# Optimization experiments

Hardware: AMD Instinct MI355X
Metric: run time of the kernel (lower is better)

The kernel has to match this reference:

```python
import jax, jax.numpy as jnp
import numpy as np

MARGIN = 0.2
EPS = 1e-6  # torch.pairwise_distance default eps added to (x1 - x2)


def setup_inputs() -> dict:
    key = jax.random.key(0)
    k1, k2 = jax.random.split(key)
    N, D = 8192, 128
    x = jax.random.normal(k1, (N, D), dtype=jnp.float32)
    target = jax.random.randint(k2, (N,), 0, 1000)
    return {"x": x, "target": target}


def _pairwise_dist(x):
    # torch.pairwise_distance(x.unsqueeze(0), x.unsqueeze(1)):
    #   diff[i, j] = x[j] - x[i] + EPS ; dist[i, j] = ||diff[i, j]||_2
    # Expanded quadratic form avoids the [N, N, D] diff tensor:
    #   ||a - b + e||^2 = ||a||^2 + ||b||^2 - 2 a.b + 2e*sum(a - b) + D*e^2
    sq = jnp.sum(x * x, axis=1)          # [N]
    s = jnp.sum(x, axis=1)               # [N]
    dot = x @ x.T                        # [N, N]
    D = x.shape[1]
    d2 = (sq[None, :] + sq[:, None] - 2.0 * dot
          + 2.0 * EPS * (s[None, :] - s[:, None]) + D * EPS * EPS)
    return jnp.sqrt(jnp.maximum(d2, 0.0))


def reference(x, target):
    N = x.shape[0]
    dist = _pairwise_dist(x)                                 # [N, N]
    same = target[None, :] == target[:, None]                # [N, N] bool
    pos_mask = (same & ~jnp.eye(N, dtype=bool)).astype(x.dtype)
    hardest_pos = jnp.max(pos_mask * dist, axis=1, keepdims=True)  # [N, 1]
    neg_mask = (~same).astype(x.dtype)
    max_neg = jnp.max(dist, axis=1, keepdims=True)           # [N, 1]
    anchor_neg = dist + max_neg * (1.0 - neg_mask)           # push positives up
    hardest_neg = jnp.min(anchor_neg, axis=1, keepdims=True) # [N, 1]
    loss = jax.nn.relu(hardest_pos - hardest_neg + MARGIN)
    return jnp.mean(loss)
```

## Files before the change

kernel.cpp:

```cpp
#include <hip/hip_runtime.h>

#define N 8192
#define Dk 128
#define EPSC 1e-6f
#define MARGIN 0.2f

typedef __attribute__((ext_vector_type(8))) short bf16x8;
typedef __attribute__((ext_vector_type(4))) float f32x4;

__device__ __forceinline__ unsigned short f2bf(float f) {
    unsigned u = __float_as_uint(f);
    u = (u + 0x7FFFu + ((u >> 16) & 1u)) >> 16;
    return (unsigned short)u;
}

__global__ void prep_kernel(const float* __restrict__ x, const int* __restrict__ tgt,
                            uint4* __restrict__ Frag, uint2* __restrict__ QT,
                            float* __restrict__ P) {
    int wv = blockIdx.x * 4 + (threadIdx.x >> 6);
    int lane = threadIdx.x & 63;
    int row = wv * 4 + (lane >> 4);
    int c = lane & 15;
    const float4* x4 = reinterpret_cast<const float4*>(x);
    float4 v0 = x4[row * 32 + c * 2];
    float4 v1 = x4[row * 32 + c * 2 + 1];
    float sq = v0.x * v0.x + v0.y * v0.y + v0.z * v0.z + v0.w * v0.w +
               v1.x * v1.x + v1.y * v1.y + v1.z * v1.z + v1.w * v1.w;
    float s = v0.x + v0.y + v0.z + v0.w + v1.x + v1.y + v1.z + v1.w;
    ushort4 lo, hi;
    lo.x = f2bf(v0.x); lo.y = f2bf(v0.y); lo.z = f2bf(v0.z); lo.w = f2bf(v0.w);
    hi.x = f2bf(v1.x); hi.y = f2bf(v1.y); hi.z = f2bf(v1.z); hi.w = f2bf(v1.w);
    uint4 pk;
    pk.x = (unsigned)lo.x | ((unsigned)lo.y << 16);
    pk.y = (unsigned)lo.z | ((unsigned)lo.w << 16);
    pk.z = (unsigned)hi.x | ((unsigned)hi.y << 16);
    pk.w = (unsigned)hi.z | ((unsigned)hi.w << 16);
    Frag[((row >> 4) * 4 + (c >> 2)) * 64 + (c & 3) * 16 + (row & 15)] = pk;
#pragma unroll
    for (int m = 1; m <= 8; m <<= 1) {
        sq += __shfl_xor(sq, m);
        s += __shfl_xor(s, m);
    }
    if (c == 0) {
        P[row] = sq - 2.0f * EPSC * s;
        float Qj = sq + 2.0f * EPSC * s + (float)Dk * EPSC * EPSC;
        uint2 qt;
        qt.x = __float_as_uint(-0.5f * Qj);
        qt.y = (unsigned)tgt[row];
        QT[row] = qt;
    }
}

#define LOADB(Bb, qq, t)                              \
    do {                                              \
        const int jt_ = jt0 + (t);                    \
        Bb[0] = Fr[(jt_ * 4 + 0) * 64 + lane];        \
        Bb[1] = Fr[(jt_ * 4 + 1) * 64 + lane];        \
        Bb[2] = Fr[(jt_ * 4 + 2) * 64 + lane];        \
        Bb[3] = Fr[(jt_ * 4 + 3) * 64 + lane];        \
        qq = QT[jt_ * 16 + n];                        \
    } while (0)

#define COMPUTE(Bb, qq)                                                               \
    do {                                                                              \
        const float Qv_ = __uint_as_float(qq.x);                        \
        const int tv_ = (int)qq.y;                                                    \
        f32x4 acc[4];                                                                 \
        acc[0] = Qv_; acc[1] = Qv_; acc[2] = Qv_; acc[3] = Qv_;                       \
        _Pragma("unroll")                                                             \
        for (int kk = 0; kk < 4; ++kk) {                                              \
            _Pragma("unroll")                                                         \
            for (int ti = 0; ti < 4; ++ti)                                            \
                acc[ti] = __builtin_amdgcn_mfma_f32_16x16x32_bf16(Af[ti][kk], Bb[kk], \
                                                                  acc[ti], 0, 0, 0);  \
        }                                                                             \
        _Pragma("unroll")                                                             \
        for (int ti = 0; ti < 4; ++ti) {                                              \
            f32x4 v = acc[ti];                                                        \
            int e0 = tv_ == tsl[4 * ti + 0];                                          \
            int e1 = tv_ == tsl[4 * ti + 1];                                          \
            int e2 = tv_ == tsl[4 * ti + 2];                                          \
            int e3 = tv_ == tsl[4 * ti + 3];                                          \
            if (__ballot(e0 | e1 | e2 | e3)) {                                        \
                hp[4 * ti + 0] = fminf(hp[4 * ti + 0], e0 ? v[0] : INFINITY);         \
                hp[4 * ti + 1] = fminf(hp[4 * ti + 1], e1 ? v[1] : INFINITY);         \
                hp[4 * ti + 2] = fminf(hp[4 * ti + 2], e2 ? v[2] : INFINITY);         \
                hp[4 * ti + 3] = fminf(hp[4 * ti + 3], e3 ? v[3] : INFINITY);         \
                mn[4 * ti + 0] = fmaxf(mn[4 * ti + 0], e0 ? -INFINITY : v[0]);        \
                mn[4 * ti + 1] = fmaxf(mn[4 * ti + 1], e1 ? -INFINITY : v[1]);        \
                mn[4 * ti + 2] = fmaxf(mn[4 * ti + 2], e2 ? -INFINITY : v[2]);        \
                mn[4 * ti + 3] = fmaxf(mn[4 * ti + 3], e3 ? -INFINITY : v[3]);        \
            } else {                                                                  \
                mn[4 * ti + 0] = fmaxf(mn[4 * ti + 0], v[0]);                         \
                mn[4 * ti + 1] = fmaxf(mn[4 * ti + 1], v[1]);                         \
                mn[4 * ti + 2] = fmaxf(mn[4 * ti + 2], v[2]);                         \
                mn[4 * ti + 3] = fmaxf(mn[4 * ti + 3], v[3]);                         \
            }                                                                         \
        }                                                                             \
    } while (0)

__global__ __launch_bounds__(256, 2) void main_kernel(
        const uint4* __restrict__ Frag, const uint2* __restrict__ QT,
        const int* __restrict__ tgt,
        float* __restrict__ partHp, float* __restrict__ partMn) {
    const int w = threadIdx.x >> 6;
    const int lane = threadIdx.x & 63;
    const int n = lane & 15;
    const int q = lane >> 4;

    const int ig = (int)blockIdx.x >> 3;
    const int jg = (int)blockIdx.x & 7;
    const int rbase = ig * 64;
    const int jt0 = jg * 64 + w * 16;

    const bf16x8* Fr = reinterpret_cast<const bf16x8*>(Frag);

    bf16x8 Af[4][4];
#pragma unroll
    for (int ti = 0; ti < 4; ++ti)
#pragma unroll
        for (int kk = 0; kk < 4; ++kk)
            Af[ti][kk] = Fr[((ig * 4 + ti) * 4 + kk) * 64 + lane];

    int tsl[16];
#pragma unroll
    for (int ti = 0; ti < 4; ++ti) {
        int4 t4 = *reinterpret_cast<const int4*>(&tgt[rbase + 16 * ti + 4 * q]);
        tsl[4 * ti + 0] = t4.x;
        tsl[4 * ti + 1] = t4.y;
        tsl[4 * ti + 2] = t4.z;
        tsl[4 * ti + 3] = t4.w;
    }

    float hp[16], mn[16];
#pragma unroll
    for (int s = 0; s < 16; ++s) {
        hp[s] = INFINITY;
        mn[s] = -INFINITY;
    }

    bf16x8 Ba[4], Bb[4], Bc[4], Bd[4];
    uint2 qa, qb, qc, qd;

    LOADB(Ba, qa, 0);
    LOADB(Bb, qb, 1);
    LOADB(Bc, qc, 2);
    LOADB(Bd, qd, 3);
#pragma unroll
    for (int tt = 0; tt < 16; tt += 4) {
        COMPUTE(Ba, qa);
        if (tt < 12) LOADB(Ba, qa, tt + 4);
        COMPUTE(Bb, qb);
        if (tt < 12) LOADB(Bb, qb, tt + 5);
        COMPUTE(Bc, qc);
        if (tt < 12) LOADB(Bc, qc, tt + 6);
        COMPUTE(Bd, qd);
        if (tt < 12) LOADB(Bd, qd, tt + 7);
    }

#pragma unroll
    for (int m = 1; m <= 8; m <<= 1) {
#pragma unroll
        for (int s = 0; s < 16; ++s) {
            hp[s] = fminf(hp[s], __shfl_xor(hp[s], m));
            mn[s] = fmaxf(mn[s], __shfl_xor(mn[s], m));
        }
    }
    if (n == 0) {
        const int wg = jg * 4 + w;
#pragma unroll
        for (int ti = 0; ti < 4; ++ti)
#pragma unroll
            for (int r = 0; r < 4; ++r) {
                int i = rbase + 16 * ti + 4 * q + r;
                partHp[wg * N + i] = hp[4 * ti + r];
                partMn[wg * N + i] = mn[4 * ti + r];
            }
    }
}

__global__ void finish_kernel(const float* __restrict__ P,
                              const float* __restrict__ partHp,
                              const float* __restrict__ partMn,
                              float* __restrict__ out) {
    int i = blockIdx.x * 256 + threadIdx.x;
    float hpm = INFINITY, mnm = -INFINITY;
#pragma unroll
    for (int wg = 0; wg < 32; ++wg) {
        hpm = fminf(hpm, partHp[wg * N + i]);
        mnm = fmaxf(mnm, partMn[wg * N + i]);
    }
    float Pi = P[i];
    float hp = sqrtf(fmaxf(fmaf(-2.0f, hpm, Pi), 0.0f));
    float hn = sqrtf(fmaxf(fmaf(-2.0f, mnm, Pi), 0.0f));
    float sum = fmaxf(hp - hn + MARGIN, 0.0f) * (1.0f / (float)N);
#pragma unroll
    for (int m = 32; m >= 1; m >>= 1) sum += __shfl_xor(sum, m);
    __shared__ float ws[4];
    int lane = threadIdx.x & 63, wv = threadIdx.x >> 6;
    if (lane == 0) ws[wv] = sum;
    __syncthreads();
    if (threadIdx.x == 0) atomicAdd(out, ws[0] + ws[1] + ws[2] + ws[3]);
}

extern "C" void kernel_launch(void* const* d_in, const int* in_sizes, int n_in,
                              void* d_out, int out_size, void* d_ws, size_t ws_size,
                              hipStream_t stream) {
    const float* x = (const float*)d_in[0];
    const int* tgt = (const int*)d_in[1];
    float* out = (float*)d_out;

    char* ws = (char*)d_ws;
    const size_t frag_b = (size_t)N * Dk * 2;
    uint4* Frag = (uint4*)ws;
    uint2* QT = (uint2*)(ws + frag_b);
    float* P = (float*)(ws + frag_b + (size_t)N * 8);
    float* partHp = (float*)(ws + frag_b + (size_t)N * 12);
    float* partMn = (float*)(ws + frag_b + (size_t)N * 12 + (size_t)32 * N * 4);

    hipMemsetAsync(d_out, 0, sizeof(float), stream);
    prep_kernel<<<N / 16, 256, 0, stream>>>(x, tgt, Frag, QT, P);
    main_kernel<<<1024, 256, 0, stream>>>(Frag, QT, tgt, partHp, partMn);
    finish_kernel<<<32, 256, 0, stream>>>(P, partHp, partMn, out);
}
```

Measured before the change: 102.0 us.

## Sort rows by class so same-class checks run only on band tiles

Adds a counting sort of samples by target class (histogram, prefix scan, scatter) and permutes the rows when building the bf16 fragments. In the main kernel each 64-row block then knows the column range that holds its own classes and runs the per-element equality and hardest-positive path only for tiles that overlap that range. All other tiles do a plain max update, which removes the per-tile compares and ballots. The price is three extra small launches plus atomics, and the B-prefetch ring shrinks from four buffers to three.

```diff
diff --git a/kernel.cpp b/kernel.cpp
--- a/kernel.cpp
+++ b/kernel.cpp
@@ -2,6 +2,7 @@
 
 #define N 8192
 #define Dk 128
+#define NC 1024
 #define EPSC 1e-6f
 #define MARGIN 0.2f
 
@@ -14,16 +15,57 @@
     return (unsigned short)u;
 }
 
-__global__ void prep_kernel(const float* __restrict__ x, const int* __restrict__ tgt,
+__global__ void hist_kernel(const int* __restrict__ tgt, int* __restrict__ hist) {
+    int i = blockIdx.x * 256 + threadIdx.x;
+    atomicAdd(&hist[tgt[i]], 1);
+}
+
+__global__ void scan_kernel(const int* __restrict__ hist, int* __restrict__ pref,
+                            int* __restrict__ cursor) {
+    __shared__ int tmp[NC];
+    int t = threadIdx.x;
+    int h = hist[t];
+    tmp[t] = h;
+    __syncthreads();
+#pragma unroll
+    for (int off = 1; off < NC; off <<= 1) {
+        int v = (t >= off) ? tmp[t - off] : 0;
+        __syncthreads();
+        tmp[t] += v;
+        __syncthreads();
+    }
+    int ex = tmp[t] - h;
+    pref[t] = ex;
+    cursor[t] = ex;
+}
+
+__global__ void scatter_kernel(const int* __restrict__ tgt, const int* __restrict__ pref,
+                               const int* __restrict__ hist, int* __restrict__ cursor,
+                               int* __restrict__ perm, uint2* __restrict__ band,
+                               int* __restrict__ cls) {
+    int i = blockIdx.x * 256 + threadIdx.x;
+    int c = tgt[i];
+    int pos = atomicAdd(&cursor[c], 1);
+    perm[pos] = i;
+    uint2 b;
+    b.x = (unsigned)pref[c];
+    b.y = (unsigned)(pref[c] + hist[c]);
+    band[pos] = b;
+    cls[pos] = c;
+}
+
+__global__ void prep_kernel(const float* __restrict__ x, const int* __restrict__ perm,
+                            const int* __restrict__ cls,
                             uint4* __restrict__ Frag, uint2* __restrict__ QT,
                             float* __restrict__ P) {
     int wv = blockIdx.x * 4 + (threadIdx.x >> 6);
     int lane = threadIdx.x & 63;
-    int row = wv * 4 + (lane >> 4);
+    int k = wv * 4 + (lane >> 4);
     int c = lane & 15;
+    int orig = perm[k];
     const float4* x4 = reinterpret_cast<const float4*>(x);
-    float4 v0 = x4[row * 32 + c * 2];
-    float4 v1 = x4[row * 32 + c * 2 + 1];
+    float4 v0 = x4[orig * 32 + c * 2];
+    float4 v1 = x4[orig * 32 + c * 2 + 1];
     float sq = v0.x * v0.x + v0.y * v0.y + v0.z * v0.z + v0.w * v0.w +
                v1.x * v1.x + v1.y * v1.y + v1.z * v1.z + v1.w * v1.w;
     float s = v0.x + v0.y + v0.z + v0.w + v1.x + v1.y + v1.z + v1.w;
@@ -35,36 +77,35 @@
     pk.y = (unsigned)lo.z | ((unsigned)lo.w << 16);
     pk.z = (unsigned)hi.x | ((unsigned)hi.y << 16);
     pk.w = (unsigned)hi.z | ((unsigned)hi.w << 16);
-    Frag[((row >> 4) * 4 + (c >> 2)) * 64 + (c & 3) * 16 + (row & 15)] = pk;
+    Frag[((k >> 4) * 4 + (c >> 2)) * 64 + (c & 3) * 16 + (k & 15)] = pk;
 #pragma unroll
     for (int m = 1; m <= 8; m <<= 1) {
         sq += __shfl_xor(sq, m);
         s += __shfl_xor(s, m);
     }
     if (c == 0) {
-        P[row] = sq - 2.0f * EPSC * s;
+        P[k] = sq - 2.0f * EPSC * s;
         float Qj = sq + 2.0f * EPSC * s + (float)Dk * EPSC * EPSC;
         uint2 qt;
         qt.x = __float_as_uint(-0.5f * Qj);
-        qt.y = (unsigned)tgt[row];
-        QT[row] = qt;
-    }
-}
-
-#define LOADB(Bb, qq, t)                              \
-    do {                                              \
-        const int jt_ = jt0 + (t);                    \
-        Bb[0] = Fr[(jt_ * 4 + 0) * 64 + lane];        \
-        Bb[1] = Fr[(jt_ * 4 + 1) * 64 + lane];        \
-        Bb[2] = Fr[(jt_ * 4 + 2) * 64 + lane];        \
-        Bb[3] = Fr[(jt_ * 4 + 3) * 64 + lane];        \
-        qq = QT[jt_ * 16 + n];                        \
+        qt.y = (unsigned)cls[k];
+        QT[k] = qt;
+    }
+}
+
+#define LOADB(Bb, qq, t)                       \
+    do {                                       \
+        const int jt_ = jt0 + (t);             \
+        Bb[0] = Fr[(jt_ * 4 + 0) * 64 + lane]; \
+        Bb[1] = Fr[(jt_ * 4 + 1) * 64 + lane]; \
+        Bb[2] = Fr[(jt_ * 4 + 2) * 64 + lane]; \
+        Bb[3] = Fr[(jt_ * 4 + 3) * 64 + lane]; \
+        qq = QT[jt_ * 16 + n];                 \
     } while (0)
 
-#define COMPUTE(Bb, qq)                                                               \
+#define COMPUTE(Bb, qq, t)                                                            \
     do {                                                                              \
         const float Qv_ = __uint_as_float(qq.x);                        \
-        const int tv_ = (int)qq.y;                                                    \
         f32x4 acc[4];                                                                 \
         acc[0] = Qv_; acc[1] = Qv_; acc[2] = Qv_; acc[3] = Qv_;                       \
         _Pragma("unroll")                                                             \
@@ -74,14 +115,16 @@
                 acc[ti] = __builtin_amdgcn_mfma_f32_16x16x32_bf16(Af[ti][kk], Bb[kk], \
                                                                   acc[ti], 0, 0, 0);  \
         }                                                                             \
-        _Pragma("unroll")                                                             \
-        for (int ti = 0; ti < 4; ++ti) {                                              \
-            f32x4 v = acc[ti];                                                        \
-            int e0 = tv_ == tsl[4 * ti + 0];                                          \
-            int e1 = tv_ == tsl[4 * ti + 1];                                          \
-            int e2 = tv_ == tsl[4 * ti + 2];                                          \
-            int e3 = tv_ == tsl[4 * ti + 3];                                          \
-            if (__ballot(e0 | e1 | e2 | e3)) {                                        \
+        const int jc_ = (jt0 + (t)) * 16;                                             \
+        if (jc_ < bHi && jc_ + 16 > bLo) {      \
+            const int tv_ = (int)qq.y;                                                \
+            _Pragma("unroll")                                                         \
+            for (int ti = 0; ti < 4; ++ti) {                                          \
+                f32x4 v = acc[ti];                                                    \
+                int e0 = tv_ == tsl[4 * ti + 0];                                      \
+                int e1 = tv_ == tsl[4 * ti + 1];                                      \
+                int e2 = tv_ == tsl[4 * ti + 2];                                      \
+                int e3 = tv_ == tsl[4 * ti + 3];                                      \
                 hp[4 * ti + 0] = fminf(hp[4 * ti + 0], e0 ? v[0] : INFINITY);         \
                 hp[4 * ti + 1] = fminf(hp[4 * ti + 1], e1 ? v[1] : INFINITY);         \
                 hp[4 * ti + 2] = fminf(hp[4 * ti + 2], e2 ? v[2] : INFINITY);         \
@@ -90,18 +133,21 @@
                 mn[4 * ti + 1] = fmaxf(mn[4 * ti + 1], e1 ? -INFINITY : v[1]);        \
                 mn[4 * ti + 2] = fmaxf(mn[4 * ti + 2], e2 ? -INFINITY : v[2]);        \
                 mn[4 * ti + 3] = fmaxf(mn[4 * ti + 3], e3 ? -INFINITY : v[3]);        \
-            } else {                                                                  \
-                mn[4 * ti + 0] = fmaxf(mn[4 * ti + 0], v[0]);                         \
-                mn[4 * ti + 1] = fmaxf(mn[4 * ti + 1], v[1]);                         \
-                mn[4 * ti + 2] = fmaxf(mn[4 * ti + 2], v[2]);                         \
-                mn[4 * ti + 3] = fmaxf(mn[4 * ti + 3], v[3]);                         \
+            }                                                                         \
+        } else {                  \
+            _Pragma("unroll")                                                         \
+            for (int ti = 0; ti < 4; ++ti) {                                          \
+                mn[4 * ti + 0] = fmaxf(mn[4 * ti + 0], acc[ti][0]);                   \
+                mn[4 * ti + 1] = fmaxf(mn[4 * ti + 1], acc[ti][1]);                   \
+                mn[4 * ti + 2] = fmaxf(mn[4 * ti + 2], acc[ti][2]);                   \
+                mn[4 * ti + 3] = fmaxf(mn[4 * ti + 3], acc[ti][3]);                   \
             }                                                                         \
         }                                                                             \
     } while (0)
 
 __global__ __launch_bounds__(256, 2) void main_kernel(
         const uint4* __restrict__ Frag, const uint2* __restrict__ QT,
-        const int* __restrict__ tgt,
+        const int* __restrict__ cls, const uint2* __restrict__ band,
         float* __restrict__ partHp, float* __restrict__ partMn) {
     const int w = threadIdx.x >> 6;
     const int lane = threadIdx.x & 63;
@@ -115,6 +161,9 @@
 
     const bf16x8* Fr = reinterpret_cast<const bf16x8*>(Frag);
 
+    const int bLo = (int)band[rbase].x;
+    const int bHi = (int)band[rbase + 63].y;
+
     bf16x8 Af[4][4];
 #pragma unroll
     for (int ti = 0; ti < 4; ++ti)
@@ -125,7 +174,7 @@
     int tsl[16];
 #pragma unroll
     for (int ti = 0; ti < 4; ++ti) {
-        int4 t4 = *reinterpret_cast<const int4*>(&tgt[rbase + 16 * ti + 4 * q]);
+        int4 t4 = *reinterpret_cast<const int4*>(&cls[rbase + 16 * ti + 4 * q]);
         tsl[4 * ti + 0] = t4.x;
         tsl[4 * ti + 1] = t4.y;
         tsl[4 * ti + 2] = t4.z;
@@ -139,24 +188,21 @@
         mn[s] = -INFINITY;
     }
 
-    bf16x8 Ba[4], Bb[4], Bc[4], Bd[4];
-    uint2 qa, qb, qc, qd;
-
-    LOADB(Ba, qa, 0);
-    LOADB(Bb, qb, 1);
-    LOADB(Bc, qc, 2);
-    LOADB(Bd, qd, 3);
-#pragma unroll
-    for (int tt = 0; tt < 16; tt += 4) {
-        COMPUTE(Ba, qa);
-        if (tt < 12) LOADB(Ba, qa, tt + 4);
-        COMPUTE(Bb, qb);
-        if (tt < 12) LOADB(Bb, qb, tt + 5);
-        COMPUTE(Bc, qc);
-        if (tt < 12) LOADB(Bc, qc, tt + 6);
-        COMPUTE(Bd, qd);
-        if (tt < 12) LOADB(Bd, qd, tt + 7);
-    }
+    bf16x8 B0[4], B1[4], B2[4];
+    uint2 q0, q1, q2;
+    LOADB(B0, q0, 0);
+    LOADB(B1, q1, 1);
+    LOADB(B2, q2, 2);
+#pragma unroll
+    for (int tt = 0; tt < 15; tt += 3) {
+        COMPUTE(B0, q0, tt);
+        if (tt + 3 < 16) LOADB(B0, q0, tt + 3);
+        COMPUTE(B1, q1, tt + 1);
+        if (tt + 4 < 16) LOADB(B1, q1, tt + 4);
+        COMPUTE(B2, q2, tt + 2);
+        if (tt + 5 < 16) LOADB(B2, q2, tt + 5);
+    }
+    COMPUTE(B0, q0, 15);
 
 #pragma unroll
     for (int m = 1; m <= 8; m <<= 1) {
@@ -211,15 +257,25 @@
     float* out = (float*)d_out;
 
     char* ws = (char*)d_ws;
-    const size_t frag_b = (size_t)N * Dk * 2;
-    uint4* Frag = (uint4*)ws;
-    uint2* QT = (uint2*)(ws + frag_b);
-    float* P = (float*)(ws + frag_b + (size_t)N * 8);
-    float* partHp = (float*)(ws + frag_b + (size_t)N * 12);
-    float* partMn = (float*)(ws + frag_b + (size_t)N * 12 + (size_t)32 * N * 4);
-
+    size_t off = 0;
+    uint4* Frag = (uint4*)(ws + off); off += (size_t)N * Dk * 2;
+    uint2* QT = (uint2*)(ws + off); off += (size_t)N * 8;
+    float* P = (float*)(ws + off); off += (size_t)N * 4;
+    float* partHp = (float*)(ws + off); off += (size_t)32 * N * 4;
+    float* partMn = (float*)(ws + off); off += (size_t)32 * N * 4;
+    uint2* band = (uint2*)(ws + off); off += (size_t)N * 8;
+    int* perm = (int*)(ws + off); off += (size_t)N * 4;
+    int* cls = (int*)(ws + off); off += (size_t)N * 4;
+    int* hist = (int*)(ws + off); off += NC * 4;
+    int* pref = (int*)(ws + off); off += NC * 4;
+    int* cursor = (int*)(ws + off); off += NC * 4;
+
+    hipMemsetAsync(hist, 0, NC * 4, stream);
     hipMemsetAsync(d_out, 0, sizeof(float), stream);
-    prep_kernel<<<N / 16, 256, 0, stream>>>(x, tgt, Frag, QT, P);
-    main_kernel<<<1024, 256, 0, stream>>>(Frag, QT, tgt, partHp, partMn);
+    hist_kernel<<<N / 256, 256, 0, stream>>>(tgt, hist);
+    scan_kernel<<<1, NC, 0, stream>>>(hist, pref, cursor);
+    scatter_kernel<<<N / 256, 256, 0, stream>>>(tgt, pref, hist, cursor, perm, band, cls);
+    prep_kernel<<<N / 16, 256, 0, stream>>>(x, perm, cls, Frag, QT, P);
+    main_kernel<<<1024, 256, 0, stream>>>(Frag, QT, cls, band, partHp, partMn);
     finish_kernel<<<32, 256, 0, stream>>>(P, partHp, partMn, out);
 }
```

Measured after the change: 105.3 us. 3.3% more time.
